# Performance work log

Measured on AMD Instinct MI355X. Metric: run time of the kernel, lower is better.

The kernel has to match this reference:

```python
import jax, jax.numpy as jnp
import numpy as np

# Constants mirroring the torch module / argparse defaults
DECAY = 0.2           # LIF membrane decay
DECAY_TRACE = 0.99    # pre-synaptic trace decay
DECAY_TRACE2 = 0.99   # post-synaptic trace decay
INH = 1.625           # lateral inhibition strength (mode='max')
A1 = 0.96             # STDP potentiation coefficient
A2 = 0.53             # STDP depression coefficient
PLUS = 0.002          # adaptive threshold increment
THR_CAP = 350.0       # threshold cap in getthresh
B, IN, OUT = 128, 8192, 4096


def setup_inputs() -> dict:
    key = jax.random.key(0)
    ks = jax.random.split(key, 7)
    x = (jax.random.uniform(ks[0], (B, IN)) < 0.1).astype(jnp.float32)
    # weight after normweight(): clamp to [0,1], scale each row so row-max == 0.1
    w = jax.random.uniform(ks[1], (OUT, IN))
    w = jnp.clip(w, 0.0, 1.0)
    w = w / (w.max(axis=1, keepdims=True) / 0.1)
    mem = jax.random.uniform(ks[2], (B, OUT)) * 10.0          # warm membrane state
    threshold = 20.0 + 40.0 * jax.random.uniform(ks[3], (OUT,))  # per-neuron adaptive threshold
    trace = jax.random.uniform(ks[4], (B, IN))                 # warm pre-trace
    trace2 = jax.random.uniform(ks[5], (B, OUT))               # warm post-trace
    wta_rand = jax.random.uniform(ks[6], (B, OUT))             # WTA random tie-breaker
    return {"x": x, "weight": w, "mem": mem, "threshold": threshold,
            "trace": trace, "trace2": trace2, "wta_rand": wta_rand,
            "time_window": 10}


def reference(x, weight, mem, threshold, trace, trace2, wta_rand, time_window):
    batch = x.shape[0]
    # linear (no bias): i = x @ W^T   [B, OUT]
    i = x @ weight.T
    # --- LIF membrane update with hard reset ---
    mem = mem * DECAY + i
    s = (mem >= threshold[None, :]).astype(x.dtype)
    mem = mem * (1.0 - s)
    # --- winner-take-all (k=1) with random tie-break among spiking neurons ---
    pos = s * wta_rand
    winner = s * (pos >= pos.max(axis=1, keepdims=True)).astype(x.dtype)
    # --- adaptive lateral inhibition (mode='max'): suppress losers' membrane ---
    any_spk = winner.max(axis=1, keepdims=True)  # rows that fired
    mem = mem - INH * i.max(axis=1, keepdims=True) * (1.0 - winner) * any_spk
    spikes = winner
    # --- STDP traces and weight updates (training path) ---
    trace2_dec = trace2 * DECAY_TRACE2               # trace2 BEFORE adding current spikes
    dw2 = jnp.einsum('bo,bi->oi', trace2_dec, x)     # post-pre depression term
    trace_new = trace * DECAY_TRACE + x              # pre-trace replaces x for dw
    dw = jnp.einsum('bo,bi->oi', spikes, trace_new)  # pre-post potentiation term
    # --- adaptive threshold balance (ATB) ---
    thr = threshold + PLUS * (i * spikes).sum(0)
    thr = thr - jnp.maximum(thr.max() - THR_CAP, 0.0)
    # accumulated STDP weight change self.dw
    dw_total = (A1 * dw - A2 * dw2) / (time_window * batch)
    return spikes, dw_total, thr, mem
```

## Files before the change

### kernel.cpp

```cpp
#include <hip/hip_runtime.h>
#include <hip/hip_bf16.h>

typedef unsigned short u16;
typedef __bf16 bf16x8 __attribute__((ext_vector_type(8)));
typedef u16   u16x4  __attribute__((ext_vector_type(4)));
typedef float f32x4  __attribute__((ext_vector_type(4)));

#define MFMA16(A,B,C) __builtin_amdgcn_mfma_f32_16x16x32_bf16(A,B,C,0,0,0)

#define B_DIM   128
#define IN_DIM  8192
#define OUT_DIM 4096

__device__ __forceinline__ u16 f2bf(float f){
  __hip_bfloat16 h = __float2bfloat16(f);
  return __builtin_bit_cast(u16, h);
}
__device__ __forceinline__ float bf2f(u16 u){
  __hip_bfloat16 h = __builtin_bit_cast(__hip_bfloat16, u);
  return __bfloat162float(h);
}

__global__ __launch_bounds__(256) void prep(const float* __restrict__ x,
    const float* __restrict__ trace, const float* __restrict__ trace2,
    const int* __restrict__ twp, u16* __restrict__ xbf,
    u16* __restrict__ Bcat, u16* __restrict__ Acat){
  __shared__ u16 s0[64*130];
  __shared__ u16 s1[64*130];
  const int tid = threadIdx.x;
  if (blockIdx.x < 128){
    const int in0 = blockIdx.x*64;
    #pragma unroll
    for (int rep=0; rep<8; ++rep){
      int flat = rep*256 + tid;
      int b = flat >> 4, i4 = (flat & 15)*4;
      size_t gi = (size_t)b*IN_DIM + in0 + i4;
      float4 xv = *reinterpret_cast<const float4*>(&x[gi]);
      float4 tv = *reinterpret_cast<const float4*>(&trace[gi]);
      u16 xb[4];
      #pragma unroll
      for (int e=0;e<4;++e){
        float xe = (&xv.x)[e];
        xb[e] = f2bf(xe);
        s0[(i4+e)*130 + b] = xb[e];
        s1[(i4+e)*130 + b] = f2bf(__fadd_rn(__fmul_rn(0.99f, (&tv.x)[e]), xe));
      }
      *reinterpret_cast<u16x4*>(&xbf[gi]) = (u16x4){xb[0],xb[1],xb[2],xb[3]};
    }
    __syncthreads();
    #pragma unroll
    for (int rep=0; rep<32; ++rep){
      int flat = rep*256 + tid;
      int row = flat >> 7, bc = flat & 127;
      size_t base = (size_t)(in0+row)*256;
      Bcat[base + bc]       = s1[row*130 + bc];
      Bcat[base + 128 + bc] = s0[row*130 + bc];
    }
  } else {
    const int o0 = (blockIdx.x - 128)*64;
    const float scale = -(0.53f*0.99f) / (float)(twp[0]*B_DIM);
    #pragma unroll
    for (int rep=0; rep<8; ++rep){
      int flat = rep*256 + tid;
      int b = flat >> 4, o4 = (flat & 15)*4;
      float4 v = *reinterpret_cast<const float4*>(&trace2[(size_t)b*OUT_DIM + o0 + o4]);
      #pragma unroll
      for (int e=0;e<4;++e) s0[(o4+e)*130 + b] = f2bf((&v.x)[e]*scale);
    }
    __syncthreads();
    #pragma unroll
    for (int rep=0; rep<32; ++rep){
      int flat = rep*256 + tid;
      int row = flat >> 7, bc = flat & 127;
      Acat[(size_t)(o0+row)*256 + 128 + bc] = s0[row*130 + bc];
    }
  }
}

__global__ __launch_bounds__(256) void t128s(const float* __restrict__ spikes,
    const int* __restrict__ twp, u16* __restrict__ Acat){
  __shared__ u16 s0[64*130];
  const int o0 = blockIdx.x*64;
  const int tid = threadIdx.x;
  const float scale = 0.96f / (float)(twp[0]*B_DIM);
  #pragma unroll
  for (int rep=0; rep<8; ++rep){
    int flat = rep*256 + tid;
    int b = flat >> 4, o4 = (flat & 15)*4;
    float4 v = *reinterpret_cast<const float4*>(&spikes[(size_t)b*OUT_DIM + o0 + o4]);
    #pragma unroll
    for (int e=0;e<4;++e) s0[(o4+e)*130 + b] = f2bf((&v.x)[e]*scale);
  }
  __syncthreads();
  #pragma unroll
  for (int rep=0; rep<32; ++rep){
    int flat = rep*256 + tid;
    int row = flat >> 7, bc = flat & 127;
    Acat[(size_t)(o0+row)*256 + bc] = s0[row*130 + bc];
  }
}

__global__ __launch_bounds__(256) void k1_gemm(const float* __restrict__ W,
    const u16* __restrict__ xbf, float* __restrict__ part){
  __shared__ __align__(16) u16 whi[32*72];
  __shared__ __align__(16) u16 wlo[32*72];
  const int n0    = blockIdx.x*32;
  const int kc    = blockIdx.y;
  const int kbase = kc*1024;
  const int tid   = threadIdx.x;
  const int lane  = tid & 63, wid = tid >> 6;
  const int m0    = wid*32;
  const int l15   = lane & 15, lg = lane >> 4;

  f32x4 acc[2][2];
  #pragma unroll
  for (int a=0;a<2;++a)
    #pragma unroll
    for (int c=0;c<2;++c){ acc[a][c][0]=0.f; acc[a][c][1]=0.f; acc[a][c][2]=0.f; acc[a][c][3]=0.f; }

  const int qr[2] = { (tid)>>4, (tid+256)>>4 };
  const int qc[2] = { (tid&15)*4, (tid&15)*4 };
  float4 wreg[2];
  #pragma unroll
  for (int j=0;j<2;++j)
    wreg[j] = *reinterpret_cast<const float4*>(
        &W[(size_t)(n0+qr[j])*IN_DIM + kbase + qc[j]]);

  for (int step=0; step<16; ++step){
    const int k0 = kbase + step*64;
    #pragma unroll
    for (int j=0;j<2;++j){
      u16 h[4], l[4];
      #pragma unroll
      for (int e=0;e<4;++e){
        float c = (&wreg[j].x)[e];
        u16 hh = f2bf(c);
        h[e] = hh;
        l[e] = f2bf(__fsub_rn(c, bf2f(hh)));
      }
      *reinterpret_cast<u16x4*>(&whi[qr[j]*72 + qc[j]]) = (u16x4){h[0],h[1],h[2],h[3]};
      *reinterpret_cast<u16x4*>(&wlo[qr[j]*72 + qc[j]]) = (u16x4){l[0],l[1],l[2],l[3]};
    }
    if (step < 15){
      #pragma unroll
      for (int j=0;j<2;++j)
        wreg[j] = *reinterpret_cast<const float4*>(
            &W[(size_t)(n0+qr[j])*IN_DIM + k0 + 64 + qc[j]]);
    }
    __syncthreads();

    bf16x8 af[2][2];
    #pragma unroll
    for (int mi=0;mi<2;++mi)
      #pragma unroll
      for (int ks=0;ks<2;++ks)
        af[mi][ks] = *reinterpret_cast<const bf16x8*>(
            &xbf[(size_t)(m0 + 16*mi + l15)*IN_DIM + k0 + ks*32 + 8*lg]);

    #pragma unroll
    for (int ni=0;ni<2;++ni){
      const int bb = (16*ni + l15)*72 + 8*lg;
      #pragma unroll
      for (int ks=0;ks<2;++ks){
        bf16x8 bh = *reinterpret_cast<const bf16x8*>(&whi[bb + ks*32]);
        bf16x8 bl = *reinterpret_cast<const bf16x8*>(&wlo[bb + ks*32]);
        acc[0][ni] = MFMA16(af[0][ks], bh, acc[0][ni]);
        acc[1][ni] = MFMA16(af[1][ks], bh, acc[1][ni]);
        acc[0][ni] = MFMA16(af[0][ks], bl, acc[0][ni]);
        acc[1][ni] = MFMA16(af[1][ks], bl, acc[1][ni]);
      }
    }
    __syncthreads();
  }
  #pragma unroll
  for (int mi=0;mi<2;++mi)
    #pragma unroll
    for (int ni=0;ni<2;++ni)
      #pragma unroll
      for (int r=0;r<4;++r){
        int row = m0 + 16*mi + 4*lg + r;
        int col = n0 + 16*ni + l15;
        part[((size_t)kc*B_DIM + row)*OUT_DIM + col] = acc[mi][ni][r];
      }
}

__global__ __launch_bounds__(512) void k2_lif(const float* __restrict__ part,
    const float* __restrict__ mem, const float* __restrict__ thr,
    const float* __restrict__ wta, float* __restrict__ spikes,
    float* __restrict__ mem_out, float* __restrict__ iacc){
  const int b = blockIdx.x;
  const int tid = threadIdx.x;
  const size_t base = (size_t)b*OUT_DIM;
  float vv[8], pv[8], ia[8];
  int sm = 0;
  float pmax = -1.f, imax = -3.4e38f;
  #pragma unroll
  for (int j=0;j<2;++j){
    const int o = 4*tid + 2048*j;
    f32x4 a = *reinterpret_cast<const f32x4*>(&part[base + o]);
    #pragma unroll
    for (int c=1;c<8;++c){
      f32x4 p4 = *reinterpret_cast<const f32x4*>(
          &part[((size_t)c*B_DIM + b)*OUT_DIM + o]);
      #pragma unroll
      for (int e=0;e<4;++e) a[e] = __fadd_rn(a[e], p4[e]);
    }
    *reinterpret_cast<f32x4*>(&iacc[base + o]) = a;
    f32x4 m4 = *reinterpret_cast<const f32x4*>(&mem[base + o]);
    f32x4 t4 = *reinterpret_cast<const f32x4*>(&thr[o]);
    f32x4 w4 = *reinterpret_cast<const f32x4*>(&wta[base + o]);
    #pragma unroll
    for (int e=0;e<4;++e){
      int idx = 4*j + e;
      float ii = a[e];
      float v  = __fadd_rn(__fmul_rn(m4[e], 0.2f), ii);
      bool  s  = (v >= t4[e]);
      float p  = s ? w4[e] : 0.f;
      ia[idx]=ii; vv[idx]=v; pv[idx]=p;
      sm |= s ? (1<<idx) : 0;
      pmax = fmaxf(pmax, p);
      imax = fmaxf(imax, ii);
    }
  }
  (void)ia;
  float anyv = (sm!=0) ? 1.f : 0.f;
  #pragma unroll
  for (int off=32; off>=1; off>>=1){
    pmax = fmaxf(pmax, __shfl_xor(pmax, off));
    imax = fmaxf(imax, __shfl_xor(imax, off));
    anyv = fmaxf(anyv, __shfl_xor(anyv, off));
  }
  __shared__ float sp[8], si[8], sa[8];
  const int wid = tid>>6, lane = tid&63;
  if (lane==0){ sp[wid]=pmax; si[wid]=imax; sa[wid]=anyv; }
  __syncthreads();
  pmax = sp[0]; imax = si[0]; anyv = sa[0];
  #pragma unroll
  for (int k=1;k<8;++k){
    pmax = fmaxf(pmax, sp[k]); imax = fmaxf(imax, si[k]); anyv = fmaxf(anyv, sa[k]);
  }
  const float isub = __fmul_rn(1.625f, imax);
  #pragma unroll
  for (int j=0;j<2;++j){
    const int o = 4*tid + 2048*j;
    f32x4 sp4, mm4;
    #pragma unroll
    for (int e=0;e<4;++e){
      int idx = 4*j + e;
      bool s   = (sm>>idx)&1;
      bool win = s && (pv[idx] >= pmax);
      sp4[e] = win ? 1.f : 0.f;
      float mv  = s ? 0.f : vv[idx];
      float sub = (anyv>0.f && !win) ? isub : 0.f;
      mm4[e] = __fsub_rn(mv, sub);
    }
    *reinterpret_cast<f32x4*>(&spikes[base + o])  = sp4;
    *reinterpret_cast<f32x4*>(&mem_out[base + o]) = mm4;
  }
}

__global__ __launch_bounds__(256) void k3a(const float* __restrict__ iacc,
    const float* __restrict__ spikes, float* __restrict__ thrpart){
  const int o  = blockIdx.x*256 + threadIdx.x;
  const int bc = blockIdx.y;
  float acc = 0.f;
  #pragma unroll
  for (int bb=0; bb<16; ++bb){
    int b = bc*16 + bb;
    acc = __fadd_rn(acc, __fmul_rn(iacc[(size_t)b*OUT_DIM+o], spikes[(size_t)b*OUT_DIM+o]));
  }
  thrpart[(size_t)bc*OUT_DIM + o] = acc;
}

__global__ __launch_bounds__(1024) void k3bc(const float* __restrict__ thrpart,
    const float* __restrict__ threshold, float* __restrict__ thr_out){
  const int tid = threadIdx.x;
  const int o = tid*4;
  f32x4 s = *reinterpret_cast<const f32x4*>(&thrpart[o]);
  #pragma unroll
  for (int c=1;c<8;++c){
    f32x4 p4 = *reinterpret_cast<const f32x4*>(&thrpart[(size_t)c*OUT_DIM + o]);
    #pragma unroll
    for (int e=0;e<4;++e) s[e] = __fadd_rn(s[e], p4[e]);
  }
  f32x4 t4 = *reinterpret_cast<const f32x4*>(&threshold[o]);
  float t0[4];
  #pragma unroll
  for (int e=0;e<4;++e) t0[e] = __fadd_rn(t4[e], __fmul_rn(0.002f, s[e]));
  float m = fmaxf(fmaxf(t0[0],t0[1]), fmaxf(t0[2],t0[3]));
  #pragma unroll
  for (int off=32; off>=1; off>>=1) m = fmaxf(m, __shfl_xor(m, off));
  __shared__ float sm16[16];
  const int wid = tid>>6, lane = tid&63;
  if (lane==0) sm16[wid] = m;
  __syncthreads();
  float g = sm16[0];
  #pragma unroll
  for (int k=1;k<16;++k) g = fmaxf(g, sm16[k]);
  float ex = fmaxf(__fsub_rn(g, 350.f), 0.f);
  f32x4 outv;
  #pragma unroll
  for (int e=0;e<4;++e) outv[e] = __fsub_rn(t0[e], ex);
  *reinterpret_cast<f32x4*>(&thr_out[o]) = outv;
}

__global__ __launch_bounds__(256) void k4_dw(const u16* __restrict__ Acat,
    const u16* __restrict__ Bcat, float* __restrict__ dw){
  const int ot = blockIdx.x;
  const int it = blockIdx.y;
  const int tid = threadIdx.x;
  const int lane = tid&63, wid = tid>>6;
  const int l15 = lane&15, lg = lane>>4;
  const int o0 = ot*64;
  const int iw = it*256 + wid*64;
  f32x4 acc[4][4];
  #pragma unroll
  for (int a=0;a<4;++a)
    #pragma unroll
    for (int c=0;c<4;++c){ acc[a][c][0]=0.f; acc[a][c][1]=0.f; acc[a][c][2]=0.f; acc[a][c][3]=0.f; }

  const size_t abase = (size_t)(o0 + l15)*256 + 8*lg;
  const size_t bbase = (size_t)(iw + l15)*256 + 8*lg;
  #pragma unroll
  for (int ks=0; ks<8; ++ks){
    const int k = ks*32;
    bf16x8 a[4], bb[4];
    #pragma unroll
    for (int mi=0;mi<4;++mi)
      a[mi] = *reinterpret_cast<const bf16x8*>(&Acat[abase + (size_t)mi*16*256 + k]);
    #pragma unroll
    for (int ni=0;ni<4;++ni)
      bb[ni] = *reinterpret_cast<const bf16x8*>(&Bcat[bbase + (size_t)ni*16*256 + k]);
    #pragma unroll
    for (int mi=0;mi<4;++mi)
      #pragma unroll
      for (int ni=0;ni<4;++ni)
        acc[mi][ni] = MFMA16(a[mi], bb[ni], acc[mi][ni]);
  }
  #pragma unroll
  for (int mi=0;mi<4;++mi)
    #pragma unroll
    for (int ni=0;ni<4;++ni)
      #pragma unroll
      for (int r=0;r<4;++r)
        dw[(size_t)(o0 + 16*mi + 4*lg + r)*IN_DIM + iw + 16*ni + l15] = acc[mi][ni][r];
}

extern "C" void kernel_launch(void* const* d_in, const int* in_sizes, int n_in,
                              void* d_out, int out_size, void* d_ws, size_t ws_size,
                              hipStream_t stream) {
  (void)in_sizes; (void)n_in; (void)out_size; (void)ws_size;
  const float* x      = (const float*)d_in[0];
  const float* weight = (const float*)d_in[1];
  const float* mem    = (const float*)d_in[2];
  const float* thresh = (const float*)d_in[3];
  const float* trace  = (const float*)d_in[4];
  const float* trace2 = (const float*)d_in[5];
  const float* wta    = (const float*)d_in[6];
  const int*   twp    = (const int*)d_in[7];

  float* out    = (float*)d_out;
  float* spikes = out;
  float* dwout  = out + 524288;
  float* throut = out + 34078720;
  float* memout = out + 34082816;

  char* ws = (char*)d_ws;
  float* iacc    = (float*)ws;
  u16*   xbf     = (u16*)(ws + (2u<<20));
  u16*   Acat    = (u16*)(ws + (4u<<20));
  u16*   Bcat    = (u16*)(ws + (6u<<20));
  float* thrpart = (float*)(ws + (10u<<20));

  float* part = dwout;

  prep <<<dim3(192),    dim3(256),  0, stream>>>(x, trace, trace2, twp, xbf, Bcat, Acat);
  k1_gemm<<<dim3(128,8),dim3(256),  0, stream>>>(weight, xbf, part);
  k2_lif<<<dim3(128),   dim3(512),  0, stream>>>(part, mem, thresh, wta, spikes, memout, iacc);
  t128s<<<dim3(64),     dim3(256),  0, stream>>>(spikes, twp, Acat);
  k3a  <<<dim3(16,8),   dim3(256),  0, stream>>>(iacc, spikes, thrpart);
  k3bc <<<dim3(1),      dim3(1024), 0, stream>>>(thrpart, thresh, throut);
  k4_dw<<<dim3(64,32),  dim3(256),  0, stream>>>(Acat, Bcat, dwout);
}
```

Baseline: 357.9 us.

## Drop LDS staging in forward GEMM and split LIF kernel for more parallelism

The forward GEMM no longer stages the fp32 weight tile through shared memory as hi/lo bf16 halves. Each wave now loads W directly from global memory in MFMA fragment layout, splits it in registers, and removes both __syncthreads per step. The grid is remapped so each block covers 32 batch rows by 128 output columns. The LIF kernel is split into two passes (k2a computes partial maxima per 1024-column chunk, k2b applies WTA and reset) to launch 512 blocks instead of 128, at the cost of an extra launch and intermediate v/p buffers. Each W element is now read by four batch-row blocks instead of one, which raises global/L2 traffic for weights.

```diff
diff --git a/kernel.cpp b/kernel.cpp
--- a/kernel.cpp
+++ b/kernel.cpp
@@ -4,6 +4,7 @@
 typedef unsigned short u16;
 typedef __bf16 bf16x8 __attribute__((ext_vector_type(8)));
 typedef u16   u16x4  __attribute__((ext_vector_type(4)));
+typedef u16   u16x8  __attribute__((ext_vector_type(8)));
 typedef float f32x4  __attribute__((ext_vector_type(4)));
 
 #define MFMA16(A,B,C) __builtin_amdgcn_mfma_f32_16x16x32_bf16(A,B,C,0,0,0)
@@ -102,14 +103,12 @@
 
 __global__ __launch_bounds__(256) void k1_gemm(const float* __restrict__ W,
     const u16* __restrict__ xbf, float* __restrict__ part){
-  __shared__ __align__(16) u16 whi[32*72];
-  __shared__ __align__(16) u16 wlo[32*72];
-  const int n0    = blockIdx.x*32;
-  const int kc    = blockIdx.y;
+  const int m0    = blockIdx.x*32;
+  const int kc    = blockIdx.z;
   const int kbase = kc*1024;
   const int tid   = threadIdx.x;
   const int lane  = tid & 63, wid = tid >> 6;
-  const int m0    = wid*32;
+  const int n0    = blockIdx.y*128 + wid*32;
   const int l15   = lane & 15, lg = lane >> 4;
 
   f32x4 acc[2][2];
@@ -118,59 +117,39 @@
     #pragma unroll
     for (int c=0;c<2;++c){ acc[a][c][0]=0.f; acc[a][c][1]=0.f; acc[a][c][2]=0.f; acc[a][c][3]=0.f; }
 
-  const int qr[2] = { (tid)>>4, (tid+256)>>4 };
-  const int qc[2] = { (tid&15)*4, (tid&15)*4 };
-  float4 wreg[2];
-  #pragma unroll
-  for (int j=0;j<2;++j)
-    wreg[j] = *reinterpret_cast<const float4*>(
-        &W[(size_t)(n0+qr[j])*IN_DIM + kbase + qc[j]]);
-
-  for (int step=0; step<16; ++step){
-    const int k0 = kbase + step*64;
-    #pragma unroll
-    for (int j=0;j<2;++j){
-      u16 h[4], l[4];
+  const u16*   a0 = &xbf[(size_t)(m0 + l15)*IN_DIM + kbase + 8*lg];
+  const u16*   a1 = &xbf[(size_t)(m0 + 16 + l15)*IN_DIM + kbase + 8*lg];
+  const float* w0 = &W[(size_t)(n0 + l15)*IN_DIM + kbase + 8*lg];
+  const float* w1 = &W[(size_t)(n0 + 16 + l15)*IN_DIM + kbase + 8*lg];
+
+  #pragma unroll 2
+  for (int s=0; s<32; ++s){
+    const int k = s*32;
+    bf16x8 af[2];
+    af[0] = *reinterpret_cast<const bf16x8*>(a0 + k);
+    af[1] = *reinterpret_cast<const bf16x8*>(a1 + k);
+    #pragma unroll
+    for (int ni=0; ni<2; ++ni){
+      const float* wp = (ni ? w1 : w0) + k;
+      float4 wa = *reinterpret_cast<const float4*>(wp);
+      float4 wb = *reinterpret_cast<const float4*>(wp + 4);
+      u16 h[8], l[8];
       #pragma unroll
       for (int e=0;e<4;++e){
-        float c = (&wreg[j].x)[e];
-        u16 hh = f2bf(c);
-        h[e] = hh;
-        l[e] = f2bf(__fsub_rn(c, bf2f(hh)));
+        float c0 = (&wa.x)[e];
+        u16 hh = f2bf(c0);
+        h[e] = hh; l[e] = f2bf(__fsub_rn(c0, bf2f(hh)));
+        float c1 = (&wb.x)[e];
+        u16 hh1 = f2bf(c1);
+        h[4+e] = hh1; l[4+e] = f2bf(__fsub_rn(c1, bf2f(hh1)));
       }
-      *reinterpret_cast<u16x4*>(&whi[qr[j]*72 + qc[j]]) = (u16x4){h[0],h[1],h[2],h[3]};
-      *reinterpret_cast<u16x4*>(&wlo[qr[j]*72 + qc[j]]) = (u16x4){l[0],l[1],l[2],l[3]};
-    }
-    if (step < 15){
-      #pragma unroll
-      for (int j=0;j<2;++j)
-        wreg[j] = *reinterpret_cast<const float4*>(
-            &W[(size_t)(n0+qr[j])*IN_DIM + k0 + 64 + qc[j]]);
-    }
-    __syncthreads();
-
-    bf16x8 af[2][2];
-    #pragma unroll
-    for (int mi=0;mi<2;++mi)
-      #pragma unroll
-      for (int ks=0;ks<2;++ks)
-        af[mi][ks] = *reinterpret_cast<const bf16x8*>(
-            &xbf[(size_t)(m0 + 16*mi + l15)*IN_DIM + k0 + ks*32 + 8*lg]);
-
-    #pragma unroll
-    for (int ni=0;ni<2;++ni){
-      const int bb = (16*ni + l15)*72 + 8*lg;
-      #pragma unroll
-      for (int ks=0;ks<2;++ks){
-        bf16x8 bh = *reinterpret_cast<const bf16x8*>(&whi[bb + ks*32]);
-        bf16x8 bl = *reinterpret_cast<const bf16x8*>(&wlo[bb + ks*32]);
-        acc[0][ni] = MFMA16(af[0][ks], bh, acc[0][ni]);
-        acc[1][ni] = MFMA16(af[1][ks], bh, acc[1][ni]);
-        acc[0][ni] = MFMA16(af[0][ks], bl, acc[0][ni]);
-        acc[1][ni] = MFMA16(af[1][ks], bl, acc[1][ni]);
-      }
-    }
-    __syncthreads();
+      bf16x8 bh = __builtin_bit_cast(bf16x8, (u16x8){h[0],h[1],h[2],h[3],h[4],h[5],h[6],h[7]});
+      bf16x8 bl = __builtin_bit_cast(bf16x8, (u16x8){l[0],l[1],l[2],l[3],l[4],l[5],l[6],l[7]});
+      acc[0][ni] = MFMA16(af[0], bh, acc[0][ni]);
+      acc[1][ni] = MFMA16(af[1], bh, acc[1][ni]);
+      acc[0][ni] = MFMA16(af[0], bl, acc[0][ni]);
+      acc[1][ni] = MFMA16(af[1], bl, acc[1][ni]);
+    }
   }
   #pragma unroll
   for (int mi=0;mi<2;++mi)
@@ -184,79 +163,95 @@
       }
 }
 
-__global__ __launch_bounds__(512) void k2_lif(const float* __restrict__ part,
+__global__ __launch_bounds__(256) void k2a(const float* __restrict__ part,
     const float* __restrict__ mem, const float* __restrict__ thr,
-    const float* __restrict__ wta, float* __restrict__ spikes,
-    float* __restrict__ mem_out, float* __restrict__ iacc){
-  const int b = blockIdx.x;
-  const int tid = threadIdx.x;
+    const float* __restrict__ wta, float* __restrict__ iacc,
+    float* __restrict__ vbuf, float* __restrict__ pbuf,
+    float* __restrict__ cm){
+  const int b  = blockIdx.x;
+  const int ch = blockIdx.y;
+  const int o  = ch*1024 + threadIdx.x*4;
   const size_t base = (size_t)b*OUT_DIM;
-  float vv[8], pv[8], ia[8];
-  int sm = 0;
-  float pmax = -1.f, imax = -3.4e38f;
-  #pragma unroll
-  for (int j=0;j<2;++j){
-    const int o = 4*tid + 2048*j;
-    f32x4 a = *reinterpret_cast<const f32x4*>(&part[base + o]);
-    #pragma unroll
-    for (int c=1;c<8;++c){
-      f32x4 p4 = *reinterpret_cast<const f32x4*>(
-          &part[((size_t)c*B_DIM + b)*OUT_DIM + o]);
-      #pragma unroll
-      for (int e=0;e<4;++e) a[e] = __fadd_rn(a[e], p4[e]);
-    }
-    *reinterpret_cast<f32x4*>(&iacc[base + o]) = a;
-    f32x4 m4 = *reinterpret_cast<const f32x4*>(&mem[base + o]);
-    f32x4 t4 = *reinterpret_cast<const f32x4*>(&thr[o]);
-    f32x4 w4 = *reinterpret_cast<const f32x4*>(&wta[base + o]);
-    #pragma unroll
-    for (int e=0;e<4;++e){
-      int idx = 4*j + e;
-      float ii = a[e];
-      float v  = __fadd_rn(__fmul_rn(m4[e], 0.2f), ii);
-      bool  s  = (v >= t4[e]);
-      float p  = s ? w4[e] : 0.f;
-      ia[idx]=ii; vv[idx]=v; pv[idx]=p;
-      sm |= s ? (1<<idx) : 0;
-      pmax = fmaxf(pmax, p);
-      imax = fmaxf(imax, ii);
-    }
-  }
-  (void)ia;
-  float anyv = (sm!=0) ? 1.f : 0.f;
+
+  f32x4 a = *reinterpret_cast<const f32x4*>(&part[base + o]);
+  #pragma unroll
+  for (int c=1;c<8;++c){
+    f32x4 p4 = *reinterpret_cast<const f32x4*>(&part[((size_t)c*B_DIM + b)*OUT_DIM + o]);
+    #pragma unroll
+    for (int e=0;e<4;++e) a[e] = __fadd_rn(a[e], p4[e]);
+  }
+  *reinterpret_cast<f32x4*>(&iacc[base + o]) = a;
+
+  f32x4 m4 = *reinterpret_cast<const f32x4*>(&mem[base + o]);
+  f32x4 t4 = *reinterpret_cast<const f32x4*>(&thr[o]);
+  f32x4 w4 = *reinterpret_cast<const f32x4*>(&wta[base + o]);
+  f32x4 v4, p4e;
+  float pmax = -3.4e38f, imax = -3.4e38f, anyv = 0.f;
+  #pragma unroll
+  for (int e=0;e<4;++e){
+    float ii = a[e];
+    float v  = __fadd_rn(__fmul_rn(m4[e], 0.2f), ii);
+    bool  s  = (v >= t4[e]);
+    v4[e]  = v;
+    p4e[e] = s ? w4[e] : -1.0f;
+    pmax = fmaxf(pmax, p4e[e]);
+    imax = fmaxf(imax, ii);
+    if (s) anyv = 1.f;
+  }
+  *reinterpret_cast<f32x4*>(&vbuf[base + o]) = v4;
+  *reinterpret_cast<f32x4*>(&pbuf[base + o]) = p4e;
+
   #pragma unroll
   for (int off=32; off>=1; off>>=1){
     pmax = fmaxf(pmax, __shfl_xor(pmax, off));
     imax = fmaxf(imax, __shfl_xor(imax, off));
     anyv = fmaxf(anyv, __shfl_xor(anyv, off));
   }
-  __shared__ float sp[8], si[8], sa[8];
-  const int wid = tid>>6, lane = tid&63;
+  __shared__ float sp[4], si[4], sa[4];
+  const int wid = threadIdx.x>>6, lane = threadIdx.x&63;
   if (lane==0){ sp[wid]=pmax; si[wid]=imax; sa[wid]=anyv; }
   __syncthreads();
-  pmax = sp[0]; imax = si[0]; anyv = sa[0];
-  #pragma unroll
-  for (int k=1;k<8;++k){
-    pmax = fmaxf(pmax, sp[k]); imax = fmaxf(imax, si[k]); anyv = fmaxf(anyv, sa[k]);
+  if (threadIdx.x==0){
+    float pm = fmaxf(fmaxf(sp[0],sp[1]), fmaxf(sp[2],sp[3]));
+    float im = fmaxf(fmaxf(si[0],si[1]), fmaxf(si[2],si[3]));
+    float an = fmaxf(fmaxf(sa[0],sa[1]), fmaxf(sa[2],sa[3]));
+    cm[(size_t)(b*4 + ch)*4 + 0] = pm;
+    cm[(size_t)(b*4 + ch)*4 + 1] = im;
+    cm[(size_t)(b*4 + ch)*4 + 2] = an;
+  }
+}
+
+__global__ __launch_bounds__(256) void k2b(const float* __restrict__ vbuf,
+    const float* __restrict__ pbuf, const float* __restrict__ cm,
+    float* __restrict__ spikes, float* __restrict__ mem_out){
+  const int b  = blockIdx.x;
+  const int ch = blockIdx.y;
+  const int o  = ch*1024 + threadIdx.x*4;
+  const size_t base = (size_t)b*OUT_DIM;
+
+  float pmax = -3.4e38f, imax = -3.4e38f, anyv = 0.f;
+  #pragma unroll
+  for (int c2=0;c2<4;++c2){
+    pmax = fmaxf(pmax, cm[(size_t)(b*4 + c2)*4 + 0]);
+    imax = fmaxf(imax, cm[(size_t)(b*4 + c2)*4 + 1]);
+    anyv = fmaxf(anyv, cm[(size_t)(b*4 + c2)*4 + 2]);
   }
   const float isub = __fmul_rn(1.625f, imax);
-  #pragma unroll
-  for (int j=0;j<2;++j){
-    const int o = 4*tid + 2048*j;
-    f32x4 sp4, mm4;
-    #pragma unroll
-    for (int e=0;e<4;++e){
-      int idx = 4*j + e;
-      bool s   = (sm>>idx)&1;
-      bool win = s && (pv[idx] >= pmax);
-      sp4[e] = win ? 1.f : 0.f;
-      float mv  = s ? 0.f : vv[idx];
-      float sub = (anyv>0.f && !win) ? isub : 0.f;
-      mm4[e] = __fsub_rn(mv, sub);
-    }
-    *reinterpret_cast<f32x4*>(&spikes[base + o])  = sp4;
-    *reinterpret_cast<f32x4*>(&mem_out[base + o]) = mm4;
-  }
+
+  f32x4 v4 = *reinterpret_cast<const f32x4*>(&vbuf[base + o]);
+  f32x4 p4 = *reinterpret_cast<const f32x4*>(&pbuf[base + o]);
+  f32x4 sp4, mm4;
+  #pragma unroll
+  for (int e=0;e<4;++e){
+    bool s   = (p4[e] >= 0.f);
+    bool win = s && (p4[e] >= pmax);
+    sp4[e] = win ? 1.f : 0.f;
+    float mv  = s ? 0.f : v4[e];
+    float sub = (anyv>0.f && !win) ? isub : 0.f;
+    mm4[e] = __fsub_rn(mv, sub);
+  }
+  *reinterpret_cast<f32x4*>(&spikes[base + o])  = sp4;
+  *reinterpret_cast<f32x4*>(&mem_out[base + o]) = mm4;
 }
 
 __global__ __launch_bounds__(256) void k3a(const float* __restrict__ iacc,
@@ -371,14 +366,18 @@
   u16*   Acat    = (u16*)(ws + (4u<<20));
   u16*   Bcat    = (u16*)(ws + (6u<<20));
   float* thrpart = (float*)(ws + (10u<<20));
+  float* cm      = (float*)(ws + (10u<<20) + (256u<<10));
+  float* vbuf    = (float*)(ws + (12u<<20));
+  float* pbuf    = (float*)(ws + (14u<<20));
 
   float* part = dwout;
 
-  prep <<<dim3(192),    dim3(256),  0, stream>>>(x, trace, trace2, twp, xbf, Bcat, Acat);
-  k1_gemm<<<dim3(128,8),dim3(256),  0, stream>>>(weight, xbf, part);
-  k2_lif<<<dim3(128),   dim3(512),  0, stream>>>(part, mem, thresh, wta, spikes, memout, iacc);
-  t128s<<<dim3(64),     dim3(256),  0, stream>>>(spikes, twp, Acat);
-  k3a  <<<dim3(16,8),   dim3(256),  0, stream>>>(iacc, spikes, thrpart);
-  k3bc <<<dim3(1),      dim3(1024), 0, stream>>>(thrpart, thresh, throut);
-  k4_dw<<<dim3(64,32),  dim3(256),  0, stream>>>(Acat, Bcat, dwout);
-}
+  prep  <<<dim3(192),     dim3(256),  0, stream>>>(x, trace, trace2, twp, xbf, Bcat, Acat);
+  k1_gemm<<<dim3(4,32,8), dim3(256),  0, stream>>>(weight, xbf, part);
+  k2a   <<<dim3(128,4),   dim3(256),  0, stream>>>(part, mem, thresh, wta, iacc, vbuf, pbuf, cm);
+  k2b   <<<dim3(128,4),   dim3(256),  0, stream>>>(vbuf, pbuf, cm, spikes, memout);
+  t128s <<<dim3(64),      dim3(256),  0, stream>>>(spikes, twp, Acat);
+  k3a   <<<dim3(16,8),    dim3(256),  0, stream>>>(iacc, spikes, thrpart);
+  k3bc  <<<dim3(1),       dim3(1024), 0, stream>>>(thrpart, thresh, throut);
+  k4_dw <<<dim3(64,32),   dim3(256),  0, stream>>>(Acat, Bcat, dwout);
+}
```

New measurement: 382.2 us. +6.8%, slower.
